# Performance work log

Measured on AMD Instinct MI355X. Metric: run time of the kernel, lower is better.

Reference implementation:

```python
import jax, jax.numpy as jnp
import numpy as np

B, C, Q, E = 32, 1024, 64, 256  # batch, max_context_len, max_question_len, embedding_size
FE = 4 * E                      # final_encoding_size (self_attention=False)


def setup_inputs() -> dict:
    key = jax.random.key(0)
    ks = jax.random.split(key, 7)
    return {
        "context": jax.random.normal(ks[0], (B, C, E), dtype=jnp.float32),
        "question": jax.random.normal(ks[1], (B, Q, E), dtype=jnp.float32),
        "context_mask": jnp.ones((B, C), dtype=jnp.float32),
        "w_question": jax.random.normal(ks[2], (E,), dtype=jnp.float32),
        "w_context": jax.random.normal(ks[3], (E,), dtype=jnp.float32),
        "w_multiple": jax.random.normal(ks[4], (E,), dtype=jnp.float32),
        "final_W": jax.random.normal(ks[5], (FE, FE), dtype=jnp.float32) * (1.0 / np.sqrt(FE)),
        "final_b": jnp.zeros((FE,), dtype=jnp.float32),
    }


def reference(context, question, context_mask, w_question, w_context, w_multiple, final_W, final_b):
    # Trilinear similarity: s[b,c,q] = <w_q, q_q> + <w_c, c_c> + <w_m, c_c * q_q>
    q_weighted = question @ w_question                 # (B, Q)
    ctx_weighted = context @ w_context                 # (B, C)
    # (question.unsqueeze(1) * context.unsqueeze(2)) @ w_multiple, computed
    # without materializing the (B, C, Q, E) intermediate:
    mult = jnp.einsum('bce,bqe->bcq', context * w_multiple, question)  # (B, C, Q)
    similarity = ctx_weighted[:, :, None] + q_weighted[:, None, :] + mult  # (B, C, Q)

    # Context-to-query attention (softmax over question dim)
    c2q_att = jnp.einsum('bcq,bqe->bce', jax.nn.softmax(similarity, axis=2), question)

    # Query-to-context attention (softmax over context dim of row-max scores)
    q2c_weights = jax.nn.softmax(jnp.max(similarity, axis=2), axis=1)   # (B, C)
    q2c_att = jnp.einsum('bc,bce->be', q2c_weights, context)            # (B, E)

    attended = jnp.concatenate(
        [context, c2q_att, context * c2q_att, context * q2c_att[:, None, :]],
        axis=2)                                                          # (B, C, 4E)

    # MaskedLinear: affine map, output rows zeroed where context_mask == 0
    out = (attended @ final_W.T + final_b) * context_mask[:, :, None]    # (B, C, 4E)
    return out
```

## Files before the change

kernel.cpp:

```cpp
#include <hip/hip_runtime.h>

#define BB 32
#define CC 1024
#define QQ 64
#define EE 256
#define FE 1024
#define MM (BB*CC)

typedef __bf16 bf16_t;
typedef bf16_t bf16x8 __attribute__((ext_vector_type(8)));
typedef float f32x4 __attribute__((ext_vector_type(4)));
typedef unsigned short u16x8 __attribute__((ext_vector_type(8)));

__device__ __forceinline__ unsigned short f2bf(float f) {
  unsigned u = __float_as_uint(f);
  u += 0x7fffu + ((u >> 16) & 1u);
  return (unsigned short)(u >> 16);
}
__device__ __forceinline__ float bf2f(unsigned short u) {
  return __uint_as_float(((unsigned)u) << 16);
}

__device__ __forceinline__ void gload_lds16(const void* g, void* l) {
  __builtin_amdgcn_global_load_lds(
      (const __attribute__((address_space(1))) unsigned int*)g,
      (__attribute__((address_space(3))) unsigned int*)l, 16, 0, 0);
}

__global__ void k_prep(const float* __restrict__ question, const float* __restrict__ w_question,
                       float* __restrict__ qw,
                       const float* __restrict__ W, unsigned short* __restrict__ Wb) {
  int bx = blockIdx.x;
  if (bx < 512) {
    int gid = bx * 256 + threadIdx.x;
    int row = gid >> 6;
    int lane = gid & 63;
    const float4 q = *(const float4*)(question + (size_t)row * EE + lane * 4);
    const float4 wq = *(const float4*)(w_question + lane * 4);
    float d = q.x*wq.x + q.y*wq.y + q.z*wq.z + q.w*wq.w;
    d += __shfl_xor(d, 1);  d += __shfl_xor(d, 2);  d += __shfl_xor(d, 4);
    d += __shfl_xor(d, 8);  d += __shfl_xor(d, 16); d += __shfl_xor(d, 32);
    if (lane == 0) qw[row] = d;
  } else {
    int i = ((bx - 512) * 256 + threadIdx.x) * 4;
    float4 v = *(const float4*)(W + i);
    ushort4 o; o.x = f2bf(v.x); o.y = f2bf(v.y); o.z = f2bf(v.z); o.w = f2bf(v.w);
    *(ushort4*)(Wb + i) = o;
  }
}

#define DOT4(acc, A, Bv) acc += A.x*Bv.x + A.y*Bv.y + A.z*Bv.z + A.w*Bv.w

__launch_bounds__(256)
__global__ void k_simpv(const float* __restrict__ ctx, const float* __restrict__ question,
                        const float* __restrict__ qw_g, const float* __restrict__ w_context,
                        const float* __restrict__ w_multiple,
                        float* __restrict__ rowmax, unsigned short* __restrict__ att) {
  __shared__ float qbuf[QQ * 132];
  __shared__ float ck[64][36];
  __shared__ unsigned short Pl[QQ][68];
  __shared__ float cwl[64];
  __shared__ float qwl[QQ];
  const int tid = threadIdx.x;
  const int b = blockIdx.y;
  const int c0 = blockIdx.x * 64;
  const int tx = tid & 15, ty = tid >> 4;

  const float* qb = question + (size_t)b * (QQ * EE);
  if (tid < QQ) qwl[tid] = qw_g[b * QQ + tid];

  const int cr = tid >> 3, er = (tid & 7) * 4;
  const float* crow0 = ctx + ((size_t)(b * CC + c0 + cr)) * EE;
  const float* crow1 = crow0 + 32 * EE;
  unsigned short* arow0 = att + ((size_t)(b * CC + c0 + cr)) * FE;
  unsigned short* arow1 = arow0 + (size_t)32 * FE;
  float s[4][4] = {{0.f}};
  float cp0 = 0.f, cp1 = 0.f;

  for (int h = 0; h < 2; ++h) {
    if (h) __syncthreads();
    for (int idx = tid * 4; idx < QQ * 128; idx += 1024) {
      int row = idx >> 7, col = idx & 127;
      *(float4*)&qbuf[row * 132 + col] = *(const float4*)(qb + (size_t)row * EE + h * 128 + col);
    }
    for (int eo2 = 0; eo2 < 128; eo2 += 32) {
      const int eo = h * 128 + eo2;
      float4 cv0 = *(const float4*)(crow0 + eo + er);
      float4 cv1 = *(const float4*)(crow1 + eo + er);
      float4 wc = *(const float4*)(w_context + eo + er);
      float4 wm = *(const float4*)(w_multiple + eo + er);
      cp0 += cv0.x*wc.x + cv0.y*wc.y + cv0.z*wc.z + cv0.w*wc.w;
      cp1 += cv1.x*wc.x + cv1.y*wc.y + cv1.z*wc.z + cv1.w*wc.w;
      ushort4 u0, u1;
      u0.x = f2bf(cv0.x); u0.y = f2bf(cv0.y); u0.z = f2bf(cv0.z); u0.w = f2bf(cv0.w);
      u1.x = f2bf(cv1.x); u1.y = f2bf(cv1.y); u1.z = f2bf(cv1.z); u1.w = f2bf(cv1.w);
      *(ushort4*)(arow0 + eo + er) = u0;
      *(ushort4*)(arow1 + eo + er) = u1;
      __syncthreads();
      float4 m0, m1;
      m0.x = cv0.x*wm.x; m0.y = cv0.y*wm.y; m0.z = cv0.z*wm.z; m0.w = cv0.w*wm.w;
      m1.x = cv1.x*wm.x; m1.y = cv1.y*wm.y; m1.z = cv1.z*wm.z; m1.w = cv1.w*wm.w;
      *(float4*)&ck[cr][er] = m0;
      *(float4*)&ck[cr + 32][er] = m1;
      __syncthreads();
#pragma unroll
      for (int ee = 0; ee < 32; ee += 4) {
        float4 a0 = *(const float4*)&ck[ty +  0][ee];
        float4 a1 = *(const float4*)&ck[ty + 16][ee];
        float4 a2 = *(const float4*)&ck[ty + 32][ee];
        float4 a3 = *(const float4*)&ck[ty + 48][ee];
        float4 b0 = *(const float4*)&qbuf[(tx +  0) * 132 + eo2 + ee];
        float4 b1 = *(const float4*)&qbuf[(tx + 16) * 132 + eo2 + ee];
        float4 b2 = *(const float4*)&qbuf[(tx + 32) * 132 + eo2 + ee];
        float4 b3 = *(const float4*)&qbuf[(tx + 48) * 132 + eo2 + ee];
        DOT4(s[0][0], a0, b0); DOT4(s[0][1], a0, b1); DOT4(s[0][2], a0, b2); DOT4(s[0][3], a0, b3);
        DOT4(s[1][0], a1, b0); DOT4(s[1][1], a1, b1); DOT4(s[1][2], a1, b2); DOT4(s[1][3], a1, b3);
        DOT4(s[2][0], a2, b0); DOT4(s[2][1], a2, b1); DOT4(s[2][2], a2, b2); DOT4(s[2][3], a2, b3);
        DOT4(s[3][0], a3, b0); DOT4(s[3][1], a3, b1); DOT4(s[3][2], a3, b2); DOT4(s[3][3], a3, b3);
      }
    }
  }
  cp0 += __shfl_xor(cp0, 1); cp0 += __shfl_xor(cp0, 2); cp0 += __shfl_xor(cp0, 4);
  cp1 += __shfl_xor(cp1, 1); cp1 += __shfl_xor(cp1, 2); cp1 += __shfl_xor(cp1, 4);
  if ((tid & 7) == 0) { cwl[cr] = cp0; cwl[cr + 32] = cp1; }
  __syncthreads();

#pragma unroll
  for (int i = 0; i < 4; ++i) {
    int c = ty + 16 * i;
    float cw = cwl[c];
    float f[4], mx = -1e30f;
#pragma unroll
    for (int j = 0; j < 4; ++j) {
      f[j] = s[i][j] + cw + qwl[tx + 16 * j];
      mx = fmaxf(mx, f[j]);
    }
    mx = fmaxf(mx, __shfl_xor(mx, 1));
    mx = fmaxf(mx, __shfl_xor(mx, 2));
    mx = fmaxf(mx, __shfl_xor(mx, 4));
    mx = fmaxf(mx, __shfl_xor(mx, 8));
    float sum = 0.f;
#pragma unroll
    for (int j = 0; j < 4; ++j) { f[j] = expf(f[j] - mx); sum += f[j]; }
    sum += __shfl_xor(sum, 1);
    sum += __shfl_xor(sum, 2);
    sum += __shfl_xor(sum, 4);
    sum += __shfl_xor(sum, 8);
    float inv = 1.f / sum;
    if (tx == 0) rowmax[(size_t)b * CC + c0 + c] = mx;
#pragma unroll
    for (int j = 0; j < 4; ++j) Pl[tx + 16 * j][c] = f2bf(f[j] * inv);
  }
  __syncthreads();

  for (int ep = 0; ep < EE; ep += 64) {
    if (ep) __syncthreads();
    {
      int q = tid >> 2, e16 = (tid & 3) * 16;
      const float* src = qb + (size_t)q * EE + ep + e16;
      *(float4*)&qbuf[q * 68 + e16 +  0] = *(const float4*)(src);
      *(float4*)&qbuf[q * 68 + e16 +  4] = *(const float4*)(src + 4);
      *(float4*)&qbuf[q * 68 + e16 +  8] = *(const float4*)(src + 8);
      *(float4*)&qbuf[q * 68 + e16 + 12] = *(const float4*)(src + 12);
    }
    __syncthreads();
    float s2[4][4] = {{0.f}};
#pragma unroll 8
    for (int q = 0; q < QQ; ++q) {
      float a0 = bf2f(Pl[q][ty +  0]);
      float a1 = bf2f(Pl[q][ty + 16]);
      float a2 = bf2f(Pl[q][ty + 32]);
      float a3 = bf2f(Pl[q][ty + 48]);
      float4 bv = *(const float4*)&qbuf[q * 68 + tx * 4];
      s2[0][0] += a0 * bv.x; s2[0][1] += a0 * bv.y; s2[0][2] += a0 * bv.z; s2[0][3] += a0 * bv.w;
      s2[1][0] += a1 * bv.x; s2[1][1] += a1 * bv.y; s2[1][2] += a1 * bv.z; s2[1][3] += a1 * bv.w;
      s2[2][0] += a2 * bv.x; s2[2][1] += a2 * bv.y; s2[2][2] += a2 * bv.z; s2[2][3] += a2 * bv.w;
      s2[3][0] += a3 * bv.x; s2[3][1] += a3 * bv.y; s2[3][2] += a3 * bv.z; s2[3][3] += a3 * bv.w;
    }
#pragma unroll
    for (int i = 0; i < 4; ++i) {
      int c = ty + 16 * i;
      size_t row = (size_t)(b * CC + c0 + c);
      unsigned short* arow = att + row * (size_t)FE;
      ushort4 cu = *(const ushort4*)(arow + ep + tx * 4);
      float cx = bf2f(cu.x), cy = bf2f(cu.y), cz = bf2f(cu.z), cw = bf2f(cu.w);
      ushort4 o1, o2;
      o1.x = f2bf(s2[i][0]);       o1.y = f2bf(s2[i][1]);       o1.z = f2bf(s2[i][2]);       o1.w = f2bf(s2[i][3]);
      o2.x = f2bf(cx * s2[i][0]);  o2.y = f2bf(cy * s2[i][1]);  o2.z = f2bf(cz * s2[i][2]);  o2.w = f2bf(cw * s2[i][3]);
      *(ushort4*)(arow + 1 * EE + ep + tx * 4) = o1;
      *(ushort4*)(arow + 2 * EE + ep + tx * 4) = o2;
    }
  }
}

__global__ void k_q2c_softmax(const float* __restrict__ rowmax, float* __restrict__ q2cw) {
  int b = blockIdx.x, tid = threadIdx.x;
  __shared__ float rbuf[4], sbuf[4];
  float4 v = *(const float4*)(rowmax + (size_t)b * CC + tid * 4);
  float m = fmaxf(fmaxf(v.x, v.y), fmaxf(v.z, v.w));
  for (int off = 1; off < 64; off <<= 1) m = fmaxf(m, __shfl_xor(m, off));
  int wv = tid >> 6;
  if ((tid & 63) == 0) rbuf[wv] = m;
  __syncthreads();
  m = fmaxf(fmaxf(rbuf[0], rbuf[1]), fmaxf(rbuf[2], rbuf[3]));
  float e0 = expf(v.x - m), e1 = expf(v.y - m), e2 = expf(v.z - m), e3 = expf(v.w - m);
  float sum = e0 + e1 + e2 + e3;
  for (int off = 1; off < 64; off <<= 1) sum += __shfl_xor(sum, off);
  if ((tid & 63) == 0) sbuf[wv] = sum;
  __syncthreads();
  sum = sbuf[0] + sbuf[1] + sbuf[2] + sbuf[3];
  float inv = 1.f / sum;
  float4 o; o.x = e0 * inv; o.y = e1 * inv; o.z = e2 * inv; o.w = e3 * inv;
  *(float4*)(q2cw + (size_t)b * CC + tid * 4) = o;
}

__global__ void k_q2c_part(const unsigned short* __restrict__ att, const float* __restrict__ w,
                           float* __restrict__ part) {
  int b = blockIdx.y, ch = blockIdx.x;
  int e = threadIdx.x;
  const unsigned short* base = att + ((size_t)(b * CC + ch * 128)) * FE + e;
  const float* wp = w + b * CC + ch * 128;
  float acc = 0.f;
#pragma unroll 4
  for (int c = 0; c < 128; ++c) acc += wp[c] * bf2f(base[(size_t)c * FE]);
  part[(b * 8 + ch) * EE + e] = acc;
}

__launch_bounds__(256, 3)
__global__ void k_gemm(const unsigned short* __restrict__ A, const unsigned short* __restrict__ Bw,
                       const float* __restrict__ part, const float* __restrict__ bias,
                       const float* __restrict__ mask, float* __restrict__ out) {
  __shared__ bf16_t As[128][32];
  __shared__ bf16_t Bs[128][32];
  __shared__ float q2cl[EE];
  const int tid = threadIdx.x;
  const int lane = tid & 63;
  const int wave = tid >> 6;
  const int wr = wave >> 1, wc = wave & 1;

  const int bid = blockIdx.x;
  const int wg = (bid & 7) * 256 + (bid >> 3);
  const int bcol = (wg & 7) * 128;
  const int brow = (wg >> 3) * 128;
  const int bb = brow >> 10;

  const int r = lane & 15, kg = lane >> 4;
  const int rk = (kg ^ ((r >> 2) & 3)) * 8;

  const int srow = tid >> 2;
  const int sgr = tid & 3;
  const int ssw = (sgr ^ ((srow >> 2) & 3)) * 8;
  const unsigned short* gA0 = A  + (size_t)(brow + srow) * FE + ssw;
  const unsigned short* gA1 = gA0 + (size_t)64 * FE;
  const unsigned short* gB0 = Bw + (size_t)(bcol + srow) * FE + ssw;
  const unsigned short* gB1 = gB0 + (size_t)64 * FE;
  bf16_t* dA0 = &As[srow][sgr * 8];
  bf16_t* dA1 = dA0 + 64 * 32;
  bf16_t* dB0 = &Bs[srow][sgr * 8];
  bf16_t* dB1 = dB0 + 64 * 32;

  {
    float a = 0.f;
#pragma unroll
    for (int ch = 0; ch < 8; ++ch) a += part[(bb * 8 + ch) * EE + tid];
    q2cl[tid] = a;
  }

  f32x4 acc[4][4] = {};

  for (int k0 = 0; k0 < FE; k0 += 32) {
    if (k0 < 768) {
      gload_lds16(gA0 + k0, dA0);
      gload_lds16(gA1 + k0, dA1);
    } else {
      const int e0 = k0 - 768;
      u16x8 va = *(const u16x8*)(gA0 + e0);
      u16x8 vb = *(const u16x8*)(gA1 + e0);
      float4 g0 = *(const float4*)&q2cl[e0 + ssw];
      float4 g1 = *(const float4*)&q2cl[e0 + ssw + 4];
      u16x8 oa, ob;
      oa[0] = f2bf(bf2f(va[0]) * g0.x); oa[1] = f2bf(bf2f(va[1]) * g0.y);
      oa[2] = f2bf(bf2f(va[2]) * g0.z); oa[3] = f2bf(bf2f(va[3]) * g0.w);
      oa[4] = f2bf(bf2f(va[4]) * g1.x); oa[5] = f2bf(bf2f(va[5]) * g1.y);
      oa[6] = f2bf(bf2f(va[6]) * g1.z); oa[7] = f2bf(bf2f(va[7]) * g1.w);
      ob[0] = f2bf(bf2f(vb[0]) * g0.x); ob[1] = f2bf(bf2f(vb[1]) * g0.y);
      ob[2] = f2bf(bf2f(vb[2]) * g0.z); ob[3] = f2bf(bf2f(vb[3]) * g0.w);
      ob[4] = f2bf(bf2f(vb[4]) * g1.x); ob[5] = f2bf(bf2f(vb[5]) * g1.y);
      ob[6] = f2bf(bf2f(vb[6]) * g1.z); ob[7] = f2bf(bf2f(vb[7]) * g1.w);
      *(u16x8*)dA0 = oa;
      *(u16x8*)dA1 = ob;
    }
    gload_lds16(gB0 + k0, dB0);
    gload_lds16(gB1 + k0, dB1);
    __syncthreads();
    bf16x8 fa[4], fb[4];
#pragma unroll
    for (int m = 0; m < 4; ++m) fa[m] = *(const bf16x8*)&As[wr * 64 + m * 16 + r][rk];
#pragma unroll
    for (int n = 0; n < 4; ++n) fb[n] = *(const bf16x8*)&Bs[wc * 64 + n * 16 + r][rk];
#pragma unroll
    for (int m = 0; m < 4; ++m)
#pragma unroll
      for (int n = 0; n < 4; ++n)
        acc[m][n] = __builtin_amdgcn_mfma_f32_16x16x32_bf16(fa[m], fb[n], acc[m][n], 0, 0, 0);
    __syncthreads();
  }

#pragma unroll
  for (int m = 0; m < 4; ++m) {
#pragma unroll
    for (int n = 0; n < 4; ++n) {
#pragma unroll
      for (int reg = 0; reg < 4; ++reg) {
        int row = brow + wr * 64 + m * 16 + kg * 4 + reg;
        int col = bcol + wc * 64 + n * 16 + r;
        out[(size_t)row * FE + col] = (acc[m][n][reg] + bias[col]) * mask[row];
      }
    }
  }
}

extern "C" void kernel_launch(void* const* d_in, const int* in_sizes, int n_in,
                              void* d_out, int out_size, void* d_ws, size_t ws_size,
                              hipStream_t stream) {
  const float* ctx  = (const float*)d_in[0];
  const float* ques = (const float*)d_in[1];
  const float* mask = (const float*)d_in[2];
  const float* w_q  = (const float*)d_in[3];
  const float* w_c  = (const float*)d_in[4];
  const float* w_m  = (const float*)d_in[5];
  const float* fW   = (const float*)d_in[6];
  const float* fb   = (const float*)d_in[7];
  float* out = (float*)d_out;

  char* ws = (char*)d_ws;
  float* qw     = (float*)(ws);
  float* rowmax = (float*)(ws + 8192);
  float* q2cw   = (float*)(ws + 139264);
  float* part   = (float*)(ws + 270336);
  unsigned short* attended = (unsigned short*)(ws + 1048576);
  unsigned short* Wb       = (unsigned short*)(ws + 68157440);

  k_prep<<<1536, 256, 0, stream>>>(ques, w_q, qw, fW, Wb);
  k_simpv<<<dim3(16, 32), 256, 0, stream>>>(ctx, ques, qw, w_c, w_m, rowmax, attended);
  k_q2c_softmax<<<32, 256, 0, stream>>>(rowmax, q2cw);
  k_q2c_part<<<dim3(8, 32), 256, 0, stream>>>(attended, q2cw, part);
  k_gemm<<<2048, 256, 0, stream>>>(attended, Wb, part, fb, mask, out);
}
```

Before: 168.2 us.

## Fold context block and q2c scaling into per-batch weights, shrink GEMM K to 768

Uses the identity context·W1ᵀ + (context*q2c)·W4ᵀ = context·(W1 + W4·diag(q2c))ᵀ. A new kernel builds a per-batch modified weight block and writes it into the unused last 256 columns of the attended buffer. The GEMM then runs with K=768 instead of 1024 and loads these per-batch weights for the first 256 K-steps. This removes a quarter of the GEMM's MFMA work and the in-loop bf16 rescaling. In exchange it adds a small extra launch, per-batch weight traffic, and bf16 rounding of the combined weights.

```diff
diff --git a/kernel.cpp b/kernel.cpp
--- a/kernel.cpp
+++ b/kernel.cpp
@@ -226,13 +226,42 @@
   part[(b * 8 + ch) * EE + e] = acc;
 }
 
+__global__ void k_wmod(const unsigned short* __restrict__ Wb, const float* __restrict__ part,
+                       unsigned short* __restrict__ att) {
+  __shared__ float q2cl[EE];
+  const int b = blockIdx.y;
+  const int t = threadIdx.x;
+  {
+    float a = 0.f;
+#pragma unroll
+    for (int ch = 0; ch < 8; ++ch) a += part[(b * 8 + ch) * EE + t];
+    q2cl[t] = a;
+  }
+  __syncthreads();
+  const int n = blockIdx.x * 8 + (t >> 5);
+  const int e = (t & 31) * 8;
+  u16x8 w1 = *(const u16x8*)(Wb + (size_t)n * FE + e);
+  u16x8 w4 = *(const u16x8*)(Wb + (size_t)n * FE + 768 + e);
+  float4 g0 = *(const float4*)&q2cl[e];
+  float4 g1 = *(const float4*)&q2cl[e + 4];
+  u16x8 o;
+  o[0] = f2bf(bf2f(w1[0]) + bf2f(w4[0]) * g0.x);
+  o[1] = f2bf(bf2f(w1[1]) + bf2f(w4[1]) * g0.y);
+  o[2] = f2bf(bf2f(w1[2]) + bf2f(w4[2]) * g0.z);
+  o[3] = f2bf(bf2f(w1[3]) + bf2f(w4[3]) * g0.w);
+  o[4] = f2bf(bf2f(w1[4]) + bf2f(w4[4]) * g1.x);
+  o[5] = f2bf(bf2f(w1[5]) + bf2f(w4[5]) * g1.y);
+  o[6] = f2bf(bf2f(w1[6]) + bf2f(w4[6]) * g1.z);
+  o[7] = f2bf(bf2f(w1[7]) + bf2f(w4[7]) * g1.w);
+  *(u16x8*)(att + ((size_t)(b * CC + n)) * FE + 768 + e) = o;
+}
+
 __launch_bounds__(256, 3)
 __global__ void k_gemm(const unsigned short* __restrict__ A, const unsigned short* __restrict__ Bw,
-                       const float* __restrict__ part, const float* __restrict__ bias,
-                       const float* __restrict__ mask, float* __restrict__ out) {
+                       const float* __restrict__ bias, const float* __restrict__ mask,
+                       float* __restrict__ out) {
   __shared__ bf16_t As[128][32];
   __shared__ bf16_t Bs[128][32];
-  __shared__ float q2cl[EE];
   const int tid = threadIdx.x;
   const int lane = tid & 63;
   const int wave = tid >> 6;
@@ -250,48 +279,29 @@
   const int srow = tid >> 2;
   const int sgr = tid & 3;
   const int ssw = (sgr ^ ((srow >> 2) & 3)) * 8;
-  const unsigned short* gA0 = A  + (size_t)(brow + srow) * FE + ssw;
+  const unsigned short* gA0 = A + (size_t)(brow + srow) * FE + ssw;
   const unsigned short* gA1 = gA0 + (size_t)64 * FE;
   const unsigned short* gB0 = Bw + (size_t)(bcol + srow) * FE + ssw;
   const unsigned short* gB1 = gB0 + (size_t)64 * FE;
+  const unsigned short* gW0 = A + (size_t)(bb * CC + bcol + srow) * FE + 768 + ssw;
+  const unsigned short* gW1 = gW0 + (size_t)64 * FE;
   bf16_t* dA0 = &As[srow][sgr * 8];
   bf16_t* dA1 = dA0 + 64 * 32;
   bf16_t* dB0 = &Bs[srow][sgr * 8];
   bf16_t* dB1 = dB0 + 64 * 32;
 
-  {
-    float a = 0.f;
-#pragma unroll
-    for (int ch = 0; ch < 8; ++ch) a += part[(bb * 8 + ch) * EE + tid];
-    q2cl[tid] = a;
-  }
-
   f32x4 acc[4][4] = {};
 
-  for (int k0 = 0; k0 < FE; k0 += 32) {
-    if (k0 < 768) {
-      gload_lds16(gA0 + k0, dA0);
-      gload_lds16(gA1 + k0, dA1);
+  for (int k0 = 0; k0 < 768; k0 += 32) {
+    gload_lds16(gA0 + k0, dA0);
+    gload_lds16(gA1 + k0, dA1);
+    if (k0 < 256) {
+      gload_lds16(gW0 + k0, dB0);
+      gload_lds16(gW1 + k0, dB1);
     } else {
-      const int e0 = k0 - 768;
-      u16x8 va = *(const u16x8*)(gA0 + e0);
-      u16x8 vb = *(const u16x8*)(gA1 + e0);
-      float4 g0 = *(const float4*)&q2cl[e0 + ssw];
-      float4 g1 = *(const float4*)&q2cl[e0 + ssw + 4];
-      u16x8 oa, ob;
-      oa[0] = f2bf(bf2f(va[0]) * g0.x); oa[1] = f2bf(bf2f(va[1]) * g0.y);
-      oa[2] = f2bf(bf2f(va[2]) * g0.z); oa[3] = f2bf(bf2f(va[3]) * g0.w);
-      oa[4] = f2bf(bf2f(va[4]) * g1.x); oa[5] = f2bf(bf2f(va[5]) * g1.y);
-      oa[6] = f2bf(bf2f(va[6]) * g1.z); oa[7] = f2bf(bf2f(va[7]) * g1.w);
-      ob[0] = f2bf(bf2f(vb[0]) * g0.x); ob[1] = f2bf(bf2f(vb[1]) * g0.y);
-      ob[2] = f2bf(bf2f(vb[2]) * g0.z); ob[3] = f2bf(bf2f(vb[3]) * g0.w);
-      ob[4] = f2bf(bf2f(vb[4]) * g1.x); ob[5] = f2bf(bf2f(vb[5]) * g1.y);
-      ob[6] = f2bf(bf2f(vb[6]) * g1.z); ob[7] = f2bf(bf2f(vb[7]) * g1.w);
-      *(u16x8*)dA0 = oa;
-      *(u16x8*)dA1 = ob;
-    }
-    gload_lds16(gB0 + k0, dB0);
-    gload_lds16(gB1 + k0, dB1);
+      gload_lds16(gB0 + k0, dB0);
+      gload_lds16(gB1 + k0, dB1);
+    }
     __syncthreads();
     bf16x8 fa[4], fb[4];
 #pragma unroll
@@ -345,5 +355,6 @@
   k_simpv<<<dim3(16, 32), 256, 0, stream>>>(ctx, ques, qw, w_c, w_m, rowmax, attended);
   k_q2c_softmax<<<32, 256, 0, stream>>>(rowmax, q2cw);
   k_q2c_part<<<dim3(8, 32), 256, 0, stream>>>(attended, q2cw, part);
-  k_gemm<<<2048, 256, 0, stream>>>(attended, Wb, part, fb, mask, out);
-}
+  k_wmod<<<dim3(128, 32), 256, 0, stream>>>(Wb, part, attended);
+  k_gemm<<<2048, 256, 0, stream>>>(attended, Wb, fb, mask, out);
+}
```

New measurement: 159.1 us. 1.06x faster.
